# Optimization experiments

Measured on AMD Instinct MI355X. Metric: run time of the kernel, lower is better.

## Reference

```python
import jax, jax.numpy as jnp
import numpy as np

HIDDEN = 2048
N_HEADS = 16
N_KV_HEADS = 8
HEAD_DIM = 128
ROTARY_DIM = 32  # int(128 * 0.25), already even
ROPE_THETA = 10000000.0
EPS = 1e-6
BATCH, SEQ = 2, 2048


def _rmsnorm(x, w, eps=EPS):
    # per-head RMSNorm over last dim; weight is zero-init, scale = 1 + w
    r = jax.lax.rsqrt(jnp.mean(x * x, axis=-1, keepdims=True) + eps)
    return x * r * (1.0 + w)


def _rope(x, positions, rotary_dim, theta):
    # x: [b, s, h, rotary_dim]; rotate-halves RoPE
    half = rotary_dim // 2
    inv_freq = 1.0 / (theta ** (jnp.arange(half, dtype=jnp.float32) / half))
    ang = positions.astype(jnp.float32)[:, :, None] * inv_freq  # [b, s, half]
    cos = jnp.cos(ang)[:, :, None, :]
    sin = jnp.sin(ang)[:, :, None, :]
    x1, x2 = x[..., :half], x[..., half:]
    return jnp.concatenate([x1 * cos - x2 * sin, x1 * sin + x2 * cos], axis=-1)


def setup_inputs() -> dict:
    key = jax.random.key(0)
    ks = jax.random.split(key, 8)
    scale = lambda fan_in: 1.0 / np.sqrt(fan_in)
    x = jax.random.normal(ks[0], (BATCH, SEQ, HIDDEN), dtype=jnp.float32)
    Wq = jax.random.normal(ks[1], (HIDDEN, N_HEADS * HEAD_DIM * 2), jnp.float32) * scale(HIDDEN)
    Wk = jax.random.normal(ks[2], (HIDDEN, N_KV_HEADS * HEAD_DIM), jnp.float32) * scale(HIDDEN)
    Wv = jax.random.normal(ks[3], (HIDDEN, N_KV_HEADS * HEAD_DIM), jnp.float32) * scale(HIDDEN)
    Wo = jax.random.normal(ks[4], (N_HEADS * HEAD_DIM, HIDDEN), jnp.float32) * scale(N_HEADS * HEAD_DIM)
    q_norm_w = jax.random.normal(ks[5], (HEAD_DIM,), jnp.float32) * 0.02
    k_norm_w = jax.random.normal(ks[6], (HEAD_DIM,), jnp.float32) * 0.02
    attention_mask = jnp.ones((BATCH, SEQ), dtype=jnp.int32)
    positions = jnp.broadcast_to(jnp.arange(SEQ, dtype=jnp.int32), (BATCH, SEQ))
    return {"x": x, "attention_mask": attention_mask, "positions": positions,
            "Wq": Wq, "Wk": Wk, "Wv": Wv, "Wo": Wo,
            "q_norm_w": q_norm_w, "k_norm_w": k_norm_w}


def reference(x, attention_mask, positions, Wq, Wk, Wv, Wo, q_norm_w, k_norm_w):
    b, s, _ = x.shape
    g = N_HEADS // N_KV_HEADS  # GQA group size

    q_all = jnp.einsum('bsh,ho->bso', x, Wq).reshape(b, s, N_HEADS, HEAD_DIM * 2)
    q, gate = jnp.split(q_all, 2, axis=-1)          # each [b,s,H,D]
    gate = gate.reshape(b, s, N_HEADS * HEAD_DIM)
    q = _rmsnorm(q, q_norm_w)
    k = _rmsnorm(jnp.einsum('bsh,ho->bso', x, Wk).reshape(b, s, N_KV_HEADS, HEAD_DIM), k_norm_w)
    v = jnp.einsum('bsh,ho->bso', x, Wv).reshape(b, s, N_KV_HEADS, HEAD_DIM)

    # partial RoPE on first ROTARY_DIM dims
    q = jnp.concatenate([_rope(q[..., :ROTARY_DIM], positions, ROTARY_DIM, ROPE_THETA), q[..., ROTARY_DIM:]], axis=-1)
    k = jnp.concatenate([_rope(k[..., :ROTARY_DIM], positions, ROTARY_DIM, ROPE_THETA), k[..., ROTARY_DIM:]], axis=-1)

    # grouped-query causal attention
    qg = q.reshape(b, s, N_KV_HEADS, g, HEAD_DIM)
    scores = jnp.einsum('bqhgd,bkhd->bhgqk', qg, k) / jnp.sqrt(jnp.float32(HEAD_DIM))
    causal = jnp.tril(jnp.ones((s, s), dtype=bool))
    key_valid = attention_mask.astype(bool)[:, None, None, None, :]  # [b,1,1,1,k]
    mask = causal[None, None, None, :, :] & key_valid
    scores = jnp.where(mask, scores, jnp.finfo(scores.dtype).min)
    probs = jax.nn.softmax(scores, axis=-1)
    attn = jnp.einsum('bhgqk,bkhd->bqhgd', probs, v).reshape(b, s, N_HEADS * HEAD_DIM)

    attn = attn * jax.nn.sigmoid(gate)
    return jnp.einsum('bso,oh->bsh', attn, Wo)
```

## Files before the change

kernel.cpp:

```cpp
#include <hip/hip_runtime.h>
#include <cstdint>

typedef __bf16  bf16;
typedef __bf16  bf16x8 __attribute__((ext_vector_type(8)));
typedef __bf16  bf16x4 __attribute__((ext_vector_type(4)));
typedef float   f32x4  __attribute__((ext_vector_type(4)));
typedef float   f32x16 __attribute__((ext_vector_type(16)));

#define GLOAD_LDS16(g, l) __builtin_amdgcn_global_load_lds( \
    (const __attribute__((address_space(1))) void*)(g),     \
    (__attribute__((address_space(3))) void*)(l), 16, 0, 0)

#define SEQ   2048
#define HID   2048
#define NH    16
#define NKV   8
#define HD    128
#define NQKV  6144
#define MTOT  4096

__device__ __forceinline__ void transw_body(const float* __restrict__ W, bf16* __restrict__ WT,
                                            int N, int n0, int k0, int t) {
    __shared__ float tile[64][65];
    int tn = t & 63, t4 = t >> 6;
    #pragma unroll
    for (int i = 0; i < 16; ++i) {
        int kk = i * 4 + t4;
        tile[kk][tn] = W[(size_t)(k0 + kk) * N + n0 + tn];
    }
    __syncthreads();
    #pragma unroll
    for (int i = 0; i < 16; ++i) {
        int nn = i * 4 + t4;
        WT[(size_t)(n0 + nn) * HID + k0 + tn] = (bf16)tile[tn][nn];
    }
}

__global__ __launch_bounds__(256) void prep_kernel(const float* __restrict__ x, bf16* __restrict__ xb,
                                                   const float* __restrict__ Wq, const float* __restrict__ Wk,
                                                   const float* __restrict__ Wv, const float* __restrict__ Wo,
                                                   bf16* __restrict__ wqkvT, bf16* __restrict__ woT) {
    int bx = blockIdx.x, t = threadIdx.x;
    if (bx < 8192) {
        int i = bx * 256 + t;
        f32x4 v = ((const f32x4*)x)[i];
        bf16x4 o;
        o[0] = (bf16)v[0]; o[1] = (bf16)v[1]; o[2] = (bf16)v[2]; o[3] = (bf16)v[3];
        ((bf16x4*)xb)[i] = o;
    } else if (bx < 8192 + 2048) {
        int idx = bx - 8192;
        transw_body(Wq, wqkvT, 4096, (idx & 63) * 64, (idx >> 6) * 64, t);
    } else if (bx < 8192 + 2048 + 512) {
        int idx = bx - (8192 + 2048);
        transw_body(Wk, wqkvT + (size_t)4096 * HID, 1024, (idx & 15) * 64, (idx >> 4) * 64, t);
    } else if (bx < 8192 + 2048 + 1024) {
        int idx = bx - (8192 + 2048 + 512);
        transw_body(Wv, wqkvT + (size_t)5120 * HID, 1024, (idx & 15) * 64, (idx >> 4) * 64, t);
    } else {
        int idx = bx - (8192 + 2048 + 1024);
        transw_body(Wo, woT, 2048, (idx & 31) * 64, (idx >> 5) * 64, t);
    }
}

template<bool OUT_BF16>
__global__ __launch_bounds__(256) void gemm_bt(const bf16* __restrict__ A, const bf16* __restrict__ Bt,
                                               void* __restrict__ C, int M, int N, int K) {
    __shared__ __align__(16) bf16 As[128 * 32];
    __shared__ __align__(16) bf16 Bs[128 * 32];
    const int tid = threadIdx.x;
    const int wave = tid >> 6, lane = tid & 63;
    const int l31 = lane & 31, half = lane >> 5;
    const int tile_n = blockIdx.x * 128, tile_m = blockIdx.y * 128;
    const int wm = (wave & 1) * 64, wn = (wave >> 1) * 64;
    f32x16 acc[2][2] = {};

    for (int k0 = 0; k0 < K; k0 += 32) {
        #pragma unroll
        for (int j = 0; j < 2; ++j) {
            int c = (j * 4 + wave) * 64 + lane;
            int row = c >> 2, kq = c & 3;
            GLOAD_LDS16(A  + (size_t)(tile_m + row) * K + k0 + kq * 8, As + (size_t)(j * 4 + wave) * 512);
            GLOAD_LDS16(Bt + (size_t)(tile_n + row) * K + k0 + kq * 8, Bs + (size_t)(j * 4 + wave) * 512);
        }
        __syncthreads();
        bf16x8 a[2][2], b[2][2];
        #pragma unroll
        for (int mt = 0; mt < 2; ++mt)
            #pragma unroll
            for (int kh = 0; kh < 2; ++kh) {
                a[mt][kh] = *(const bf16x8*)(As + (size_t)(wm + mt * 32 + l31) * 32 + kh * 16 + half * 8);
                b[mt][kh] = *(const bf16x8*)(Bs + (size_t)(wn + mt * 32 + l31) * 32 + kh * 16 + half * 8);
            }
        #pragma unroll
        for (int mt = 0; mt < 2; ++mt)
            #pragma unroll
            for (int nt = 0; nt < 2; ++nt)
                #pragma unroll
                for (int kh = 0; kh < 2; ++kh)
                    acc[mt][nt] = __builtin_amdgcn_mfma_f32_32x32x16_bf16(a[mt][kh], b[nt][kh], acc[mt][nt], 0, 0, 0);
        __syncthreads();
    }
    #pragma unroll
    for (int mt = 0; mt < 2; ++mt)
        #pragma unroll
        for (int nt = 0; nt < 2; ++nt)
            #pragma unroll
            for (int reg = 0; reg < 16; ++reg) {
                int row = tile_m + wm + mt * 32 + (reg & 3) + ((reg >> 2) * 8) + half * 4;
                int col = tile_n + wn + nt * 32 + l31;
                float v = acc[mt][nt][reg];
                if (OUT_BF16) ((bf16*)C)[(size_t)row * N + col] = (bf16)v;
                else          ((float*)C)[(size_t)row * N + col] = v;
            }
}

__global__ __launch_bounds__(256) void post_kernel(const bf16* __restrict__ qkv,
                                                   const float* __restrict__ qnw, const float* __restrict__ knw,
                                                   const int* __restrict__ positions,
                                                   bf16* __restrict__ Qh, bf16* __restrict__ Kh,
                                                   bf16* __restrict__ VT) {
    int bx = blockIdx.x;
    if (bx < 4096) {
        int tk = bx;
        int b = tk >> 11, s = tk & 2047;
        int wave = threadIdx.x >> 6, lane = threadIdx.x & 63;
        float pos = (float)positions[tk];
        int fi = lane & 15;
        float ang = pos * exp2f(-(float)fi * 1.4533435415278355f);
        float cv = cosf(ang), sv = sinf(ang);

        #pragma unroll
        for (int i = 0; i < 4; ++i) {
            int h = wave + i * 4;
            const bf16* base = qkv + (size_t)tk * NQKV + h * 256;
            float v0 = (float)base[lane], v1 = (float)base[lane + 64];
            float ssq = v0 * v0 + v1 * v1;
            #pragma unroll
            for (int off = 32; off; off >>= 1) ssq += __shfl_xor(ssq, off);
            float rn = rsqrtf(ssq * (1.0f / 128.0f) + 1e-6f);
            float q0 = v0 * rn * (1.0f + qnw[lane]);
            float q1 = v1 * rn * (1.0f + qnw[lane + 64]);
            float other = __shfl_xor(q0, 16);
            float q0r = q0;
            if (lane < 16)      q0r = q0 * cv - other * sv;
            else if (lane < 32) q0r = other * sv + q0 * cv;
            bf16* qout = Qh + ((size_t)(b * NH + h) * SEQ + s) * HD;
            qout[lane] = (bf16)q0r; qout[lane + 64] = (bf16)q1;
        }
        #pragma unroll
        for (int i = 0; i < 2; ++i) {
            int h = wave + i * 4;
            const bf16* base = qkv + (size_t)tk * NQKV + 4096 + h * HD;
            float v0 = (float)base[lane], v1 = (float)base[lane + 64];
            float ssq = v0 * v0 + v1 * v1;
            #pragma unroll
            for (int off = 32; off; off >>= 1) ssq += __shfl_xor(ssq, off);
            float rn = rsqrtf(ssq * (1.0f / 128.0f) + 1e-6f);
            float k0 = v0 * rn * (1.0f + knw[lane]);
            float k1 = v1 * rn * (1.0f + knw[lane + 64]);
            float other = __shfl_xor(k0, 16);
            float k0r = k0;
            if (lane < 16)      k0r = k0 * cv - other * sv;
            else if (lane < 32) k0r = other * sv + k0 * cv;
            bf16* kout = Kh + ((size_t)(b * NKV + h) * SEQ + s) * HD;
            kout[lane] = (bf16)k0r; kout[lane + 64] = (bf16)k1;
        }
    } else {
        int idx = bx - 4096;
        int bh = idx >> 5, st = idx & 31;
        int b = bh >> 3, h = bh & 7;
        __shared__ float tile[64][129];
        int t = threadIdx.x;
        const bf16* src = qkv + ((size_t)(b * SEQ) + st * 64) * NQKV + 5120 + h * HD;
        #pragma unroll
        for (int i = 0; i < 32; ++i) {
            int ii = i * 256 + t;
            int tok = ii >> 7, d = ii & 127;
            tile[tok][d] = (float)src[(size_t)tok * NQKV + d];
        }
        __syncthreads();
        bf16* dst = VT + (size_t)(b * NKV + h) * HD * SEQ + st * 64;
        #pragma unroll
        for (int i = 0; i < 32; ++i) {
            int ii = i * 256 + t;
            int d = ii >> 6, sx = ii & 63;
            dst[(size_t)d * SEQ + sx] = (bf16)tile[sx][d];
        }
    }
}

__global__ __launch_bounds__(256, 4) void attn_kernel(const bf16* __restrict__ Qh, const bf16* __restrict__ Kh,
                                                      const bf16* __restrict__ VT, const bf16* __restrict__ qkv,
                                                      const int* __restrict__ amask, bf16* __restrict__ attnb) {
    const int bx = blockIdx.x;
    const int hb = bx >> 5;
    const int head = hb & 15, b = hb >> 4;
    const int qt = ((bx & 31) + hb) & 31;
    const int kvh = head >> 1;
    __shared__ __align__(16) bf16 Ks[64 * 128];
    __shared__ __align__(16) bf16 Vs[128 * 64];
    __shared__ __align__(16) bf16 Ps[4 * 16 * 64];
    const int tid = threadIdx.x, wave = tid >> 6, lane = tid & 63;
    const int quad = lane >> 4, cl = lane & 15;

    const bf16* qsrc = Qh + ((size_t)(b * NH + head) * SEQ + qt * 64) * HD;
    bf16x8 aq[4];
    #pragma unroll
    for (int kc = 0; kc < 4; ++kc)
        aq[kc] = *(const bf16x8*)(qsrc + (size_t)(wave * 16 + cl) * HD + kc * 32 + quad * 8);

    float mstate[4], lstate[4];
    f32x4 oacc[8] = {};
    #pragma unroll
    for (int r = 0; r < 4; ++r) { mstate[r] = -1e30f; lstate[r] = 0.0f; }
    const int qrow_glob = qt * 64 + wave * 16 + quad * 4;
    const float scale = 0.08838834764831845f * 1.4426950408889634f;

    for (int kt = 0; kt <= qt; ++kt) {
        __syncthreads();
        const bf16* ksrc = Kh + ((size_t)(b * NKV + kvh) * SEQ + kt * 64) * HD;
        const bf16* vsrc = VT + (size_t)(b * NKV + kvh) * HD * SEQ + kt * 64;
        #pragma unroll
        for (int j = 0; j < 4; ++j) {
            int s = (j * 4 + wave) * 64 + lane;
            int rK = s >> 4, cK = s & 15;
            GLOAD_LDS16(ksrc + (size_t)rK * HD + ((cK ^ (rK & 15)) << 3), Ks + (size_t)s * 8);
            int dV = s >> 3, cV = s & 7;
            GLOAD_LDS16(vsrc + (size_t)dV * SEQ + ((cV ^ (dV & 7)) << 3), Vs + (size_t)s * 8);
        }
        __syncthreads();

        f32x4 sc[4] = {};
        #pragma unroll
        for (int nt = 0; nt < 4; ++nt)
            #pragma unroll
            for (int kc = 0; kc < 4; ++kc) {
                bf16x8 bk = *(const bf16x8*)(Ks + (size_t)(nt * 16 + cl) * 128 + (((kc * 4 + quad) ^ cl) << 3));
                sc[nt] = __builtin_amdgcn_mfma_f32_16x16x32_bf16(aq[kc], bk, sc[nt], 0, 0, 0);
            }

        bool colok[4];
        int kcolb[4];
        #pragma unroll
        for (int nt = 0; nt < 4; ++nt) {
            kcolb[nt] = kt * 64 + nt * 16 + cl;
            colok[nt] = (amask[b * SEQ + kcolb[nt]] != 0);
        }
        const bool diag = (kt == qt);

        float alpha[4];
        #pragma unroll
        for (int r = 0; r < 4; ++r) {
            float rv[4];
            float tmax = -1e30f;
            #pragma unroll
            for (int nt = 0; nt < 4; ++nt) {
                float v = sc[nt][r] * scale;
                bool ok = colok[nt] && (!diag || (kcolb[nt] <= qrow_glob + r));
                v = ok ? v : -1e30f;
                rv[nt] = v;
                tmax = fmaxf(tmax, v);
            }
            #pragma unroll
            for (int off = 8; off; off >>= 1) tmax = fmaxf(tmax, __shfl_xor(tmax, off));
            float mnew = fmaxf(mstate[r], tmax);
            float al = exp2f(mstate[r] - mnew);
            mstate[r] = mnew; alpha[r] = al;
            float rsum = 0.0f;
            int prow = quad * 4 + r;
            #pragma unroll
            for (int nt = 0; nt < 4; ++nt) {
                float p = exp2f(rv[nt] - mnew);
                rsum += p;
                Ps[wave * 1024 + prow * 64 + ((nt * 16 + cl) ^ (quad << 4))] = (bf16)p;
            }
            #pragma unroll
            for (int off = 8; off; off >>= 1) rsum += __shfl_xor(rsum, off);
            lstate[r] = lstate[r] * al + rsum;
        }
        #pragma unroll
        for (int n2 = 0; n2 < 8; ++n2)
            #pragma unroll
            for (int r = 0; r < 4; ++r) oacc[n2][r] *= alpha[r];

        bf16x8 ap[2];
        #pragma unroll
        for (int c = 0; c < 2; ++c)
            ap[c] = *(const bf16x8*)(Ps + wave * 1024 + cl * 64 + ((c * 32 + quad * 8) ^ ((cl >> 2) << 4)));
        #pragma unroll
        for (int n2 = 0; n2 < 8; ++n2)
            #pragma unroll
            for (int c = 0; c < 2; ++c) {
                bf16x8 bv = *(const bf16x8*)(Vs + (size_t)(n2 * 16 + cl) * 64 + (((c * 4 + quad) ^ (cl & 7)) << 3));
                oacc[n2] = __builtin_amdgcn_mfma_f32_16x16x32_bf16(ap[c], bv, oacc[n2], 0, 0, 0);
            }
    }

    #pragma unroll
    for (int r = 0; r < 4; ++r) {
        int srow = qt * 64 + wave * 16 + quad * 4 + r;
        float linv = 1.0f / lstate[r];
        #pragma unroll
        for (int n2 = 0; n2 < 8; ++n2) {
            int d = n2 * 16 + cl;
            float g = (float)qkv[(size_t)(b * SEQ + srow) * NQKV + head * 256 + 128 + d];
            float sig = 1.0f / (1.0f + __expf(-g));
            float v = oacc[n2][r] * linv * sig;
            attnb[(size_t)(b * SEQ + srow) * HID + head * HD + d] = (bf16)v;
        }
    }
}

extern "C" void kernel_launch(void* const* d_in, const int* in_sizes, int n_in,
                              void* d_out, int out_size, void* d_ws, size_t ws_size,
                              hipStream_t stream) {
    const float* x        = (const float*)d_in[0];
    const int*   amask    = (const int*)d_in[1];
    const int*   positions= (const int*)d_in[2];
    const float* Wq       = (const float*)d_in[3];
    const float* Wk       = (const float*)d_in[4];
    const float* Wv       = (const float*)d_in[5];
    const float* Wo       = (const float*)d_in[6];
    const float* qnw      = (const float*)d_in[7];
    const float* knw      = (const float*)d_in[8];
    float* out = (float*)d_out;
    char* ws = (char*)d_ws;

    bf16* xb    = (bf16*)(ws);
    bf16* wqkvT = (bf16*)(ws + 16777216);
    bf16* woT   = (bf16*)(ws + 41943040);
    bf16* qkv   = (bf16*)(ws + 50331648);
    bf16* Qh    = (bf16*)(ws + 100663296);
    bf16* Kh    = (bf16*)(ws + 117440512);
    bf16* VT    = (bf16*)(ws + 125829120);
    bf16* attnb = (bf16*)(ws + 134217728);

    prep_kernel<<<12288, 256, 0, stream>>>(x, xb, Wq, Wk, Wv, Wo, wqkvT, woT);
    gemm_bt<true><<<dim3(48, 32), 256, 0, stream>>>(xb, wqkvT, qkv, MTOT, NQKV, HID);
    post_kernel<<<4608, 256, 0, stream>>>(qkv, qnw, knw, positions, Qh, Kh, VT);
    attn_kernel<<<1024, 256, 0, stream>>>(Qh, Kh, VT, qkv, amask, attnb);
    gemm_bt<false><<<dim3(16, 32), 256, 0, stream>>>(attnb, woT, out, MTOT, HID, HID);

    (void)in_sizes; (void)n_in; (void)out_size; (void)ws_size;
}
```

Baseline: 481.4 us.

## Double query rows per attention block and swizzle GEMM LDS tiles

The attention kernel now processes 128 query rows per block (two 64-row fragments per wave), so each K/V tile loaded into LDS feeds twice as many MFMAs. This halves the grid and reduces global K/V traffic, at the cost of more registers (occupancy hint lowered from 4 to 3) and fewer blocks. The GEMM kernel also XOR-swizzles the 16-byte chunks in its LDS tiles to reduce bank conflicts on the fragment reads.

```diff
diff --git a/kernel.cpp b/kernel.cpp
--- a/kernel.cpp
+++ b/kernel.cpp
@@ -72,6 +72,7 @@
     const int l31 = lane & 31, half = lane >> 5;
     const int tile_n = blockIdx.x * 128, tile_m = blockIdx.y * 128;
     const int wm = (wave & 1) * 64, wn = (wave >> 1) * 64;
+    const int sw = (l31 >> 1) & 3;
     f32x16 acc[2][2] = {};
 
     for (int k0 = 0; k0 < K; k0 += 32) {
@@ -79,8 +80,9 @@
         for (int j = 0; j < 2; ++j) {
             int c = (j * 4 + wave) * 64 + lane;
             int row = c >> 2, kq = c & 3;
-            GLOAD_LDS16(A  + (size_t)(tile_m + row) * K + k0 + kq * 8, As + (size_t)(j * 4 + wave) * 512);
-            GLOAD_LDS16(Bt + (size_t)(tile_n + row) * K + k0 + kq * 8, Bs + (size_t)(j * 4 + wave) * 512);
+            int kqs = kq ^ ((row >> 1) & 3);
+            GLOAD_LDS16(A  + (size_t)(tile_m + row) * K + k0 + kqs * 8, As + (size_t)(j * 4 + wave) * 512);
+            GLOAD_LDS16(Bt + (size_t)(tile_n + row) * K + k0 + kqs * 8, Bs + (size_t)(j * 4 + wave) * 512);
         }
         __syncthreads();
         bf16x8 a[2][2], b[2][2];
@@ -88,8 +90,9 @@
         for (int mt = 0; mt < 2; ++mt)
             #pragma unroll
             for (int kh = 0; kh < 2; ++kh) {
-                a[mt][kh] = *(const bf16x8*)(As + (size_t)(wm + mt * 32 + l31) * 32 + kh * 16 + half * 8);
-                b[mt][kh] = *(const bf16x8*)(Bs + (size_t)(wn + mt * 32 + l31) * 32 + kh * 16 + half * 8);
+                int ch = ((kh * 2 + half) ^ sw) << 3;
+                a[mt][kh] = *(const bf16x8*)(As + (size_t)(wm + mt * 32 + l31) * 32 + ch);
+                b[mt][kh] = *(const bf16x8*)(Bs + (size_t)(wn + mt * 32 + l31) * 32 + ch);
             }
         #pragma unroll
         for (int mt = 0; mt < 2; ++mt)
@@ -189,34 +192,38 @@
     }
 }
 
-__global__ __launch_bounds__(256, 4) void attn_kernel(const bf16* __restrict__ Qh, const bf16* __restrict__ Kh,
+__global__ __launch_bounds__(256, 3) void attn_kernel(const bf16* __restrict__ Qh, const bf16* __restrict__ Kh,
                                                       const bf16* __restrict__ VT, const bf16* __restrict__ qkv,
                                                       const int* __restrict__ amask, bf16* __restrict__ attnb) {
     const int bx = blockIdx.x;
-    const int hb = bx >> 5;
+    const int hb = bx >> 4;
     const int head = hb & 15, b = hb >> 4;
-    const int qt = ((bx & 31) + hb) & 31;
+    const int qt = ((bx & 15) + hb) & 15;
     const int kvh = head >> 1;
     __shared__ __align__(16) bf16 Ks[64 * 128];
     __shared__ __align__(16) bf16 Vs[128 * 64];
-    __shared__ __align__(16) bf16 Ps[4 * 16 * 64];
+    __shared__ __align__(16) bf16 Ps[8 * 16 * 64];
     const int tid = threadIdx.x, wave = tid >> 6, lane = tid & 63;
     const int quad = lane >> 4, cl = lane & 15;
 
-    const bf16* qsrc = Qh + ((size_t)(b * NH + head) * SEQ + qt * 64) * HD;
-    bf16x8 aq[4];
-    #pragma unroll
-    for (int kc = 0; kc < 4; ++kc)
-        aq[kc] = *(const bf16x8*)(qsrc + (size_t)(wave * 16 + cl) * HD + kc * 32 + quad * 8);
-
-    float mstate[4], lstate[4];
-    f32x4 oacc[8] = {};
-    #pragma unroll
-    for (int r = 0; r < 4; ++r) { mstate[r] = -1e30f; lstate[r] = 0.0f; }
-    const int qrow_glob = qt * 64 + wave * 16 + quad * 4;
+    const bf16* qsrc = Qh + ((size_t)(b * NH + head) * SEQ + qt * 128) * HD;
+    bf16x8 aq[2][4];
+    #pragma unroll
+    for (int rf = 0; rf < 2; ++rf)
+        #pragma unroll
+        for (int kc = 0; kc < 4; ++kc)
+            aq[rf][kc] = *(const bf16x8*)(qsrc + (size_t)(rf * 64 + wave * 16 + cl) * HD + kc * 32 + quad * 8);
+
+    float mstate[2][4], lstate[2][4];
+    f32x4 oacc[2][8] = {};
+    #pragma unroll
+    for (int rf = 0; rf < 2; ++rf)
+        #pragma unroll
+        for (int r = 0; r < 4; ++r) { mstate[rf][r] = -1e30f; lstate[rf][r] = 0.0f; }
     const float scale = 0.08838834764831845f * 1.4426950408889634f;
-
-    for (int kt = 0; kt <= qt; ++kt) {
+    const int kmax = 2 * qt + 1;
+
+    for (int kt = 0; kt <= kmax; ++kt) {
         __syncthreads();
         const bf16* ksrc = Kh + ((size_t)(b * NKV + kvh) * SEQ + kt * 64) * HD;
         const bf16* vsrc = VT + (size_t)(b * NKV + kvh) * HD * SEQ + kt * 64;
@@ -230,13 +237,14 @@
         }
         __syncthreads();
 
-        f32x4 sc[4] = {};
+        f32x4 sc[2][4] = {};
         #pragma unroll
         for (int nt = 0; nt < 4; ++nt)
             #pragma unroll
             for (int kc = 0; kc < 4; ++kc) {
                 bf16x8 bk = *(const bf16x8*)(Ks + (size_t)(nt * 16 + cl) * 128 + (((kc * 4 + quad) ^ cl) << 3));
-                sc[nt] = __builtin_amdgcn_mfma_f32_16x16x32_bf16(aq[kc], bk, sc[nt], 0, 0, 0);
+                sc[0][nt] = __builtin_amdgcn_mfma_f32_16x16x32_bf16(aq[0][kc], bk, sc[0][nt], 0, 0, 0);
+                sc[1][nt] = __builtin_amdgcn_mfma_f32_16x16x32_bf16(aq[1][kc], bk, sc[1][nt], 0, 0, 0);
             }
 
         bool colok[4];
@@ -246,69 +254,78 @@
             kcolb[nt] = kt * 64 + nt * 16 + cl;
             colok[nt] = (amask[b * SEQ + kcolb[nt]] != 0);
         }
-        const bool diag = (kt == qt);
-
-        float alpha[4];
-        #pragma unroll
-        for (int r = 0; r < 4; ++r) {
-            float rv[4];
-            float tmax = -1e30f;
-            #pragma unroll
-            for (int nt = 0; nt < 4; ++nt) {
-                float v = sc[nt][r] * scale;
-                bool ok = colok[nt] && (!diag || (kcolb[nt] <= qrow_glob + r));
-                v = ok ? v : -1e30f;
-                rv[nt] = v;
-                tmax = fmaxf(tmax, v);
-            }
-            #pragma unroll
-            for (int off = 8; off; off >>= 1) tmax = fmaxf(tmax, __shfl_xor(tmax, off));
-            float mnew = fmaxf(mstate[r], tmax);
-            float al = exp2f(mstate[r] - mnew);
-            mstate[r] = mnew; alpha[r] = al;
-            float rsum = 0.0f;
-            int prow = quad * 4 + r;
-            #pragma unroll
-            for (int nt = 0; nt < 4; ++nt) {
-                float p = exp2f(rv[nt] - mnew);
-                rsum += p;
-                Ps[wave * 1024 + prow * 64 + ((nt * 16 + cl) ^ (quad << 4))] = (bf16)p;
-            }
-            #pragma unroll
-            for (int off = 8; off; off >>= 1) rsum += __shfl_xor(rsum, off);
-            lstate[r] = lstate[r] * al + rsum;
-        }
-        #pragma unroll
-        for (int n2 = 0; n2 < 8; ++n2)
-            #pragma unroll
-            for (int r = 0; r < 4; ++r) oacc[n2][r] *= alpha[r];
-
-        bf16x8 ap[2];
-        #pragma unroll
-        for (int c = 0; c < 2; ++c)
-            ap[c] = *(const bf16x8*)(Ps + wave * 1024 + cl * 64 + ((c * 32 + quad * 8) ^ ((cl >> 2) << 4)));
+
+        #pragma unroll
+        for (int rf = 0; rf < 2; ++rf) {
+            const int qbase = qt * 128 + rf * 64 + wave * 16 + quad * 4;
+            const bool maybe_diag = (kt * 64 + 63) > qbase;
+            float alpha[4];
+            #pragma unroll
+            for (int r = 0; r < 4; ++r) {
+                float rv[4];
+                float tmax = -1e30f;
+                #pragma unroll
+                for (int nt = 0; nt < 4; ++nt) {
+                    float v = sc[rf][nt][r] * scale;
+                    bool ok = colok[nt] && (!maybe_diag || (kcolb[nt] <= qbase + r));
+                    v = ok ? v : -1e30f;
+                    rv[nt] = v;
+                    tmax = fmaxf(tmax, v);
+                }
+                #pragma unroll
+                for (int off = 8; off; off >>= 1) tmax = fmaxf(tmax, __shfl_xor(tmax, off));
+                float mnew = fmaxf(mstate[rf][r], tmax);
+                float al = exp2f(mstate[rf][r] - mnew);
+                mstate[rf][r] = mnew; alpha[r] = al;
+                float rsum = 0.0f;
+                int prow = quad * 4 + r;
+                #pragma unroll
+                for (int nt = 0; nt < 4; ++nt) {
+                    float p = exp2f(rv[nt] - mnew);
+                    rsum += p;
+                    Ps[(wave * 2 + rf) * 1024 + prow * 64 + ((nt * 16 + cl) ^ (quad << 4))] = (bf16)p;
+                }
+                #pragma unroll
+                for (int off = 8; off; off >>= 1) rsum += __shfl_xor(rsum, off);
+                lstate[rf][r] = lstate[rf][r] * al + rsum;
+            }
+            #pragma unroll
+            for (int n2 = 0; n2 < 8; ++n2)
+                #pragma unroll
+                for (int r = 0; r < 4; ++r) oacc[rf][n2][r] *= alpha[r];
+        }
+
+        bf16x8 ap[2][2];
+        #pragma unroll
+        for (int rf = 0; rf < 2; ++rf)
+            #pragma unroll
+            for (int c = 0; c < 2; ++c)
+                ap[rf][c] = *(const bf16x8*)(Ps + (wave * 2 + rf) * 1024 + cl * 64 + ((c * 32 + quad * 8) ^ ((cl >> 2) << 4)));
         #pragma unroll
         for (int n2 = 0; n2 < 8; ++n2)
             #pragma unroll
             for (int c = 0; c < 2; ++c) {
                 bf16x8 bv = *(const bf16x8*)(Vs + (size_t)(n2 * 16 + cl) * 64 + (((c * 4 + quad) ^ (cl & 7)) << 3));
-                oacc[n2] = __builtin_amdgcn_mfma_f32_16x16x32_bf16(ap[c], bv, oacc[n2], 0, 0, 0);
-            }
-    }
-
-    #pragma unroll
-    for (int r = 0; r < 4; ++r) {
-        int srow = qt * 64 + wave * 16 + quad * 4 + r;
-        float linv = 1.0f / lstate[r];
-        #pragma unroll
-        for (int n2 = 0; n2 < 8; ++n2) {
-            int d = n2 * 16 + cl;
-            float g = (float)qkv[(size_t)(b * SEQ + srow) * NQKV + head * 256 + 128 + d];
-            float sig = 1.0f / (1.0f + __expf(-g));
-            float v = oacc[n2][r] * linv * sig;
-            attnb[(size_t)(b * SEQ + srow) * HID + head * HD + d] = (bf16)v;
-        }
-    }
+                oacc[0][n2] = __builtin_amdgcn_mfma_f32_16x16x32_bf16(ap[0][c], bv, oacc[0][n2], 0, 0, 0);
+                oacc[1][n2] = __builtin_amdgcn_mfma_f32_16x16x32_bf16(ap[1][c], bv, oacc[1][n2], 0, 0, 0);
+            }
+    }
+
+    #pragma unroll
+    for (int rf = 0; rf < 2; ++rf)
+        #pragma unroll
+        for (int r = 0; r < 4; ++r) {
+            int srow = qt * 128 + rf * 64 + wave * 16 + quad * 4 + r;
+            float linv = 1.0f / lstate[rf][r];
+            #pragma unroll
+            for (int n2 = 0; n2 < 8; ++n2) {
+                int d = n2 * 16 + cl;
+                float g = (float)qkv[(size_t)(b * SEQ + srow) * NQKV + head * 256 + 128 + d];
+                float sig = 1.0f / (1.0f + __expf(-g));
+                float v = oacc[rf][n2][r] * linv * sig;
+                attnb[(size_t)(b * SEQ + srow) * HID + head * HD + d] = (bf16)v;
+            }
+        }
 }
 
 extern "C" void kernel_launch(void* const* d_in, const int* in_sizes, int n_in,
@@ -338,7 +355,7 @@
     prep_kernel<<<12288, 256, 0, stream>>>(x, xb, Wq, Wk, Wv, Wo, wqkvT, woT);
     gemm_bt<true><<<dim3(48, 32), 256, 0, stream>>>(xb, wqkvT, qkv, MTOT, NQKV, HID);
     post_kernel<<<4608, 256, 0, stream>>>(qkv, qnw, knw, positions, Qh, Kh, VT);
-    attn_kernel<<<1024, 256, 0, stream>>>(Qh, Kh, VT, qkv, amask, attnb);
+    attn_kernel<<<512, 256, 0, stream>>>(Qh, Kh, VT, qkv, amask, attnb);
     gemm_bt<false><<<dim3(16, 32), 256, 0, stream>>>(attnb, woT, out, MTOT, HID, HID);
 
     (void)in_sizes; (void)n_in; (void)out_size; (void)ws_size;
```

Result: slower. 617.7 us (+28.3%).
